# Kernel tuning notes

Hardware: AMD Instinct MI355X
Metric: run time of the kernel (lower is better)

The kernel has to match this reference:

```python
import jax, jax.numpy as jnp
import numpy as np


def setup_inputs() -> dict:
    key = jax.random.key(0)
    ks = jax.random.split(key, 7)
    T, B, D, H, F = 1024, 128, 256, 256, 128
    inputs = jax.random.normal(ks[0], (T, B, D), dtype=jnp.float32)
    # stacked gate linears (forget, input, update, output): [D+H, 4H]
    Wg = jax.random.normal(ks[1], (D + H, 4 * H), dtype=jnp.float32) / np.sqrt(D + H)
    bg = jax.random.normal(ks[2], (4 * H,), dtype=jnp.float32) * 0.01
    # stacked per-gate FFNs: Linear(H->F), ReLU, Linear(F->H), sigmoid/tanh
    W1 = jax.random.normal(ks[3], (4, H, F), dtype=jnp.float32) / np.sqrt(H)
    b1 = jax.random.normal(ks[4], (4, F), dtype=jnp.float32) * 0.01
    W2 = jax.random.normal(ks[5], (4, F, H), dtype=jnp.float32) / np.sqrt(F)
    b2 = jax.random.normal(ks[6], (4, H), dtype=jnp.float32) * 0.01
    return {"inputs": inputs, "Wg": Wg, "bg": bg, "W1": W1, "b1": b1, "W2": W2, "b2": b2}


def reference(inputs, Wg, bg, W1, b1, W2, b2):
    T, B, D = inputs.shape
    H = W2.shape[-1]

    def step(carry, x):
        hx, cx = carry
        comb = jnp.concatenate([x, hx], axis=1)              # [B, D+H]
        z = (comb @ Wg + bg).reshape(B, 4, H)                # stacked gate linears
        z = jnp.transpose(z, (1, 0, 2))                      # [4, B, H]
        h1 = jax.nn.relu(jnp.einsum('gbh,ghf->gbf', z, W1) + b1[:, None, :])
        z2 = jnp.einsum('gbf,gfh->gbh', h1, W2) + b2[:, None, :]  # [4, B, H]
        f = jax.nn.sigmoid(z2[0])
        i = jax.nn.sigmoid(z2[1])
        g = jnp.tanh(z2[2])
        o = jax.nn.sigmoid(z2[3])
        cx = f * cx + i * g
        hx = o * jnp.tanh(cx)
        return (hx, cx), hx

    h0 = jnp.zeros((B, H), dtype=inputs.dtype)
    c0 = jnp.zeros((B, H), dtype=inputs.dtype)
    (hx, cx), outputs = jax.lax.scan(step, (h0, c0), inputs)
    return outputs, (hx, cx)
```

## Files before the change

### kernel.cpp

```cpp
#include <hip/hip_runtime.h>
#include <hip/hip_fp16.h>
#include <cstdint>

#define T_STEPS 1024
#define BATCH   128
#define DIM     256
#define HID     256
#define FF      128
#define CHUNK   16

typedef _Float16 h2 __attribute__((ext_vector_type(2)));

#define WGXP_OFF 0
#define WGHP_OFF 262144
#define W1P_OFF  524288
#define W2P_OFF  655360
#define WS_HALFS 786432
#define EX_BYTE_OFF 1572864
#define EX_WORDS    262144
#define WS_SPLIT4_BYTES (EX_BYTE_OFF + EX_WORDS * 4)

#define KEEPU4(v) asm volatile("" : "+v"((v).x), "+v"((v).y), "+v"((v).z), "+v"((v).w))

__device__ __forceinline__ float sigmoidf_(float x) {
    return 1.0f / (1.0f + __expf(-x));
}
__device__ __forceinline__ float tanhf_(float x) {
    float e = __expf(2.0f * x);
    return 1.0f - 2.0f / (e + 1.0f);
}
__device__ __forceinline__ float fdot2_(h2 a, h2 b, float c) {
#if __has_builtin(__builtin_amdgcn_fdot2)
    return __builtin_amdgcn_fdot2(a, b, c, false);
#else
    return fmaf((float)a.x, (float)b.x, fmaf((float)a.y, (float)b.y, c));
#endif
}

union U4H { uint4 u; h2 h[4]; };
union HU  { unsigned short u; _Float16 h; };

__global__ __launch_bounds__(256)
void convert_kernel(const float* __restrict__ Wg,
                    const float* __restrict__ W1,
                    const float* __restrict__ W2,
                    _Float16* __restrict__ ws)
{
    int i = blockIdx.x * 256 + threadIdx.x;
    if (i < 524288) {
        int k = i >> 10, c = i & 1023;
        if (k < 256) {
            ws[WGXP_OFF + (((size_t)(k >> 3) << 10) + c) * 8 + (k & 7)] = (_Float16)Wg[i];
        } else {
            int k2 = k - 256;
            ws[WGHP_OFF + (((size_t)(k2 >> 3) << 10) + c) * 8 + (k2 & 7)] = (_Float16)Wg[i];
        }
    } else if (i < 655360) {
        int j = i - 524288;
        int g = j >> 15, k = (j >> 7) & 255, f = j & 127;
        ws[W1P_OFF + (((size_t)((g << 5) + (k >> 3)) << 7) + f) * 8 + (k & 7)] = (_Float16)W1[j];
    } else if (i < 786432) {
        int j = i - 655360;
        int g = j >> 15, f = (j >> 8) & 127, h = j & 255;
        ws[W2P_OFF + (((size_t)((g << 4) + (f >> 3)) << 8) + h) * 8 + (f & 7)] = (_Float16)W2[j];
    }
}

__global__ __launch_bounds__(512)
void exinit_kernel(unsigned* __restrict__ ex) {
    int i = blockIdx.x * 512 + threadIdx.x;
    if (i < EX_WORDS) ex[i] = 0u;
}

__global__ __launch_bounds__(512, 1)
void qlstm_split4r_kernel(const float* __restrict__ x,
                          const _Float16* __restrict__ ws,
                          unsigned* ex,
                          const float* __restrict__ bg,
                          const float* __restrict__ b1,
                          const float* __restrict__ b2,
                          float* __restrict__ out)
{
    const int blk = blockIdx.x;
    const int g   = blk >> 6;
    const int bp  = blk & 63;
    const int tid = threadIdx.x;

    __shared__ __align__(16) _Float16 xc[2 * CHUNK * DIM];
    __shared__ __align__(16) _Float16 zxc[2 * CHUNK * 256];
    __shared__ __align__(16) _Float16 ch2buf[512];
    __shared__ __align__(16) _Float16 zh[512];
    __shared__ __align__(16) _Float16 h1h[256];
    __shared__ float pbuf[1024];
    __shared__ float bgs[256], b2s[256], b1s[128];

    if (tid < 256) {
        bgs[tid] = bg[(g << 8) + tid];
        b2s[tid] = b2[(g << 8) + tid];
    }
    if (tid < 128) b1s[tid] = b1[(g << 7) + tid];
    ch2buf[tid] = (_Float16)0.0f;
    float c_reg = 0.0f;

    const uint4* __restrict__ wgxp = reinterpret_cast<const uint4*>(ws + WGXP_OFF);
    const uint4* __restrict__ wghp = reinterpret_cast<const uint4*>(ws + WGHP_OFF);
    const uint4* __restrict__ w1p  = reinterpret_cast<const uint4*>(ws + W1P_OFF);
    const uint4* __restrict__ w2p  = reinterpret_cast<const uint4*>(ws + W2P_OFF);

    const int cc   = tid & 255;
    const int kh16 = (tid >> 8) << 4;
    const int kq8  = ((tid >> 7) & 3) << 3;
    const int ffi  = tid & 127;
    const int fh8  = (tid >> 8) << 3;

    uint4 wgh_r[16], w1_r[8], w2_r[8];
    #pragma unroll
    for (int j = 0; j < 16; ++j) wgh_r[j] = wghp[((kh16 + j) << 10) + (g << 8) + cc];
    #pragma unroll
    for (int j = 0; j < 8; ++j)  w1_r[j]  = w1p[(((g << 5) + kq8 + j) << 7) + ffi];
    #pragma unroll
    for (int j = 0; j < 8; ++j)  w2_r[j]  = w2p[(((g << 4) + fh8 + j) << 8) + cc];
    #pragma unroll
    for (int j = 0; j < 16; ++j) KEEPU4(wgh_r[j]);
    #pragma unroll
    for (int j = 0; j < 8; ++j)  KEEPU4(w1_r[j]);
    #pragma unroll
    for (int j = 0; j < 8; ++j)  KEEPU4(w2_r[j]);

    __syncthreads();

    for (int t0 = 0; t0 < T_STEPS; t0 += CHUNK) {
        #pragma unroll
        for (int j = 0; j < 4; ++j) {
            int i4 = j * 512 + tid;
            int bl = i4 >> 10, rem = i4 & 1023, tl = rem >> 6, d4 = rem & 63;
            float4 v = reinterpret_cast<const float4*>(
                x + ((size_t)(t0 + tl) * BATCH + bp + (bl << 6)) * DIM)[d4];
            int base = bl * 4096 + tl * 256 + (d4 << 2);
            xc[base + 0] = (_Float16)v.x;
            xc[base + 1] = (_Float16)v.y;
            xc[base + 2] = (_Float16)v.z;
            xc[base + 3] = (_Float16)v.w;
        }
        __syncthreads();

        {
            const int th = tid >> 8;
            const U4H* xcv = reinterpret_cast<const U4H*>(xc);
            float acc[2][8];
            #pragma unroll
            for (int bl = 0; bl < 2; ++bl)
                #pragma unroll
                for (int j = 0; j < 8; ++j) acc[bl][j] = bgs[cc];
            for (int k8 = 0; k8 < 32; ++k8) {
                U4H w; w.u = wgxp[(k8 << 10) + (g << 8) + cc];
                #pragma unroll
                for (int bl = 0; bl < 2; ++bl) {
                    #pragma unroll
                    for (int j = 0; j < 8; ++j) {
                        U4H xv; xv.u = xcv[bl * 512 + (th * 8 + j) * 32 + k8].u;
                        acc[bl][j] = fdot2_(xv.h[0], w.h[0], acc[bl][j]);
                        acc[bl][j] = fdot2_(xv.h[1], w.h[1], acc[bl][j]);
                        acc[bl][j] = fdot2_(xv.h[2], w.h[2], acc[bl][j]);
                        acc[bl][j] = fdot2_(xv.h[3], w.h[3], acc[bl][j]);
                    }
                }
            }
            #pragma unroll
            for (int bl = 0; bl < 2; ++bl)
                #pragma unroll
                for (int j = 0; j < 8; ++j)
                    zxc[bl * 4096 + (th * 8 + j) * 256 + cc] = (_Float16)acc[bl][j];
        }
        __syncthreads();

        for (int tc = 0; tc < CHUNK; ++tc) {
            const int s = t0 + tc;

            {
                const uint4* hA4 = reinterpret_cast<const uint4*>(ch2buf);
                const uint4* hB4 = reinterpret_cast<const uint4*>(ch2buf + 256);
                float aA = 0.0f, aB = 0.0f;
                #pragma unroll
                for (int j = 0; j < 16; ++j) {
                    const int k8 = kh16 + j;
                    U4H w;  w.u  = wgh_r[j];
                    U4H ha; ha.u = hA4[k8];
                    U4H hb; hb.u = hB4[k8];
                    aA = fdot2_(ha.h[0], w.h[0], aA);
                    aA = fdot2_(ha.h[1], w.h[1], aA);
                    aA = fdot2_(ha.h[2], w.h[2], aA);
                    aA = fdot2_(ha.h[3], w.h[3], aA);
                    aB = fdot2_(hb.h[0], w.h[0], aB);
                    aB = fdot2_(hb.h[1], w.h[1], aB);
                    aB = fdot2_(hb.h[2], w.h[2], aB);
                    aB = fdot2_(hb.h[3], w.h[3], aB);
                }
                pbuf[tid] = aA;
                pbuf[512 + tid] = aB;
            }
            __syncthreads();
            {
                const int bl = tid >> 8, c = tid & 255;
                float z = (float)zxc[bl * 4096 + tc * 256 + c]
                        + pbuf[bl * 512 + c] + pbuf[bl * 512 + 256 + c];
                zh[bl * 256 + c] = (_Float16)z;
            }
            __syncthreads();

            {
                const uint4* zA4 = reinterpret_cast<const uint4*>(zh);
                const uint4* zB4 = reinterpret_cast<const uint4*>(zh + 256);
                float aA = 0.0f, aB = 0.0f;
                #pragma unroll
                for (int j = 0; j < 8; ++j) {
                    const int k8 = kq8 + j;
                    U4H w;  w.u  = w1_r[j];
                    U4H za; za.u = zA4[k8];
                    U4H zb; zb.u = zB4[k8];
                    aA = fdot2_(za.h[0], w.h[0], aA);
                    aA = fdot2_(za.h[1], w.h[1], aA);
                    aA = fdot2_(za.h[2], w.h[2], aA);
                    aA = fdot2_(za.h[3], w.h[3], aA);
                    aB = fdot2_(zb.h[0], w.h[0], aB);
                    aB = fdot2_(zb.h[1], w.h[1], aB);
                    aB = fdot2_(zb.h[2], w.h[2], aB);
                    aB = fdot2_(zb.h[3], w.h[3], aB);
                }
                pbuf[tid] = aA;
                pbuf[512 + tid] = aB;
            }
            __syncthreads();
            if (tid < 256) {
                const int bl = tid >> 7, f = tid & 127;
                float v = b1s[f] + pbuf[bl * 512 + f] + pbuf[bl * 512 + 128 + f]
                                 + pbuf[bl * 512 + 256 + f] + pbuf[bl * 512 + 384 + f];
                h1h[bl * 128 + f] = (_Float16)fmaxf(v, 0.0f);
            }
            __syncthreads();

            {
                const uint4* pA4 = reinterpret_cast<const uint4*>(h1h);
                const uint4* pB4 = reinterpret_cast<const uint4*>(h1h + 128);
                float aA = 0.0f, aB = 0.0f;
                #pragma unroll
                for (int j = 0; j < 8; ++j) {
                    const int f8 = fh8 + j;
                    U4H w;  w.u  = w2_r[j];
                    U4H ha; ha.u = pA4[f8];
                    U4H hb; hb.u = pB4[f8];
                    aA = fdot2_(ha.h[0], w.h[0], aA);
                    aA = fdot2_(ha.h[1], w.h[1], aA);
                    aA = fdot2_(ha.h[2], w.h[2], aA);
                    aA = fdot2_(ha.h[3], w.h[3], aA);
                    aB = fdot2_(hb.h[0], w.h[0], aB);
                    aB = fdot2_(hb.h[1], w.h[1], aB);
                    aB = fdot2_(hb.h[2], w.h[2], aB);
                    aB = fdot2_(hb.h[3], w.h[3], aB);
                }
                pbuf[tid] = aA;
                pbuf[512 + tid] = aB;
            }
            __syncthreads();

            {
                const int bl = tid >> 8, c = tid & 255;
                const int b  = bp + (bl << 6);
                float z2 = b2s[c] + pbuf[bl * 512 + c] + pbuf[bl * 512 + 256 + c];
                HU hu; hu.h = (_Float16)z2;
                unsigned word = ((unsigned)(s + 1) << 16) | (unsigned)hu.u;
                unsigned widx = (unsigned)(b * 2048 + g * 512 + ((s & 1) << 8) + c);
                __hip_atomic_store(&ex[widx], word, __ATOMIC_RELAXED, __HIP_MEMORY_SCOPE_AGENT);

                const unsigned base = (unsigned)(b * 2048 + ((s & 1) << 8) + c);
                const unsigned want = (unsigned)(s + 1) << 16;
                unsigned w0, w1, w2, w3;
                for (;;) {
                    w0 = __hip_atomic_load(&ex[base],        __ATOMIC_RELAXED, __HIP_MEMORY_SCOPE_AGENT);
                    w1 = __hip_atomic_load(&ex[base + 512],  __ATOMIC_RELAXED, __HIP_MEMORY_SCOPE_AGENT);
                    w2 = __hip_atomic_load(&ex[base + 1024], __ATOMIC_RELAXED, __HIP_MEMORY_SCOPE_AGENT);
                    w3 = __hip_atomic_load(&ex[base + 1536], __ATOMIC_RELAXED, __HIP_MEMORY_SCOPE_AGENT);
                    unsigned m = ((w0 ^ want) | (w1 ^ want) | (w2 ^ want) | (w3 ^ want)) & 0xFFFF0000u;
                    if (m == 0u) break;
                    __builtin_amdgcn_s_sleep(1);
                }
                HU hf, hi, hg, ho;
                hf.u = (unsigned short)(w0 & 0xFFFFu);
                hi.u = (unsigned short)(w1 & 0xFFFFu);
                hg.u = (unsigned short)(w2 & 0xFFFFu);
                ho.u = (unsigned short)(w3 & 0xFFFFu);
                float fg = sigmoidf_((float)hf.h);
                float ig = sigmoidf_((float)hi.h);
                float gg = tanhf_((float)hg.h);
                float og = sigmoidf_((float)ho.h);
                c_reg = fmaf(fg, c_reg, ig * gg);
                float hh = og * tanhf_(c_reg);
                ch2buf[bl * 256 + c] = (_Float16)hh;
                if (g == 0) {
                    out[((size_t)s * BATCH + b) * HID + c] = hh;
                    if (s == T_STEPS - 1) {
                        const size_t TBH = (size_t)T_STEPS * BATCH * HID;
                        out[TBH + (size_t)b * HID + c] = hh;
                        out[TBH + (size_t)BATCH * HID + (size_t)b * HID + c] = c_reg;
                    }
                }
            }
            __syncthreads();
        }
    }
}

__global__ __launch_bounds__(1024)
void qlstm_chunk_kernel(const float* __restrict__ x,
                        const _Float16* __restrict__ ws,
                        const float* __restrict__ bg,
                        const float* __restrict__ b1,
                        const float* __restrict__ b2,
                        float* __restrict__ out)
{
    const int b   = blockIdx.x;
    const int tid = threadIdx.x;

    __shared__ __align__(16) _Float16 xc[CHUNK * DIM];
    __shared__ __align__(16) _Float16 zxc[CHUNK * 1024];
    __shared__ __align__(16) _Float16 zh[1024];
    __shared__ __align__(16) _Float16 h1h[512];
    __shared__ __align__(16) _Float16 ch2buf[HID];
    __shared__ float z2buf[1024];
    __shared__ float cbuf[HID];
    __shared__ float hbuf[HID];

    const float rbg = bg[tid];
    const float rb1 = (tid < 512) ? b1[tid] : 0.0f;
    const float rb2 = b2[tid];

    if (tid < HID) { cbuf[tid] = 0.0f; hbuf[tid] = 0.0f; ch2buf[tid] = (_Float16)0.0f; }

    const uint4* __restrict__ wgxp = reinterpret_cast<const uint4*>(ws + WGXP_OFF);
    const uint4* __restrict__ wghp = reinterpret_cast<const uint4*>(ws + WGHP_OFF);
    const uint4* __restrict__ w1p  = reinterpret_cast<const uint4*>(ws + W1P_OFF);
    const uint4* __restrict__ w2p  = reinterpret_cast<const uint4*>(ws + W2P_OFF);
    const h2* ch2 = reinterpret_cast<const h2*>(ch2buf);
    const U4H* xcv = reinterpret_cast<const U4H*>(xc);

    for (int t0 = 0; t0 < T_STEPS; t0 += CHUNK) {
        #pragma unroll
        for (int j = 0; j < (CHUNK * DIM) / 1024; ++j) {
            int idx = tid + j * 1024;
            int tl = idx >> 8, d = idx & 255;
            xc[tl * DIM + d] = (_Float16)x[((size_t)(t0 + tl) * BATCH + b) * DIM + d];
        }
        __syncthreads();

        {
            float acc[CHUNK];
            #pragma unroll
            for (int tc = 0; tc < CHUNK; ++tc) acc[tc] = rbg;
            for (int k8 = 0; k8 < DIM / 8; ++k8) {
                U4H w; w.u = wgxp[(k8 << 10) + tid];
                #pragma unroll
                for (int tc = 0; tc < CHUNK; ++tc) {
                    U4H xv; xv.u = xcv[tc * (DIM / 8) + k8].u;
                    acc[tc] = fdot2_(xv.h[0], w.h[0], acc[tc]);
                    acc[tc] = fdot2_(xv.h[1], w.h[1], acc[tc]);
                    acc[tc] = fdot2_(xv.h[2], w.h[2], acc[tc]);
                    acc[tc] = fdot2_(xv.h[3], w.h[3], acc[tc]);
                }
            }
            #pragma unroll
            for (int tc = 0; tc < CHUNK; ++tc) zxc[tc * 1024 + tid] = (_Float16)acc[tc];
        }
        __syncthreads();

        for (int tc = 0; tc < CHUNK; ++tc) {
            {
                float acc = (float)zxc[tc * 1024 + tid];
                #pragma unroll 8
                for (int k8 = 0; k8 < HID / 8; ++k8) {
                    U4H w; w.u = wghp[(k8 << 10) + tid];
                    acc = fdot2_(ch2[4 * k8 + 0], w.h[0], acc);
                    acc = fdot2_(ch2[4 * k8 + 1], w.h[1], acc);
                    acc = fdot2_(ch2[4 * k8 + 2], w.h[2], acc);
                    acc = fdot2_(ch2[4 * k8 + 3], w.h[3], acc);
                }
                zh[tid] = (_Float16)acc;
            }
            __syncthreads();

            if (tid < 512) {
                const int g = tid >> 7, f = tid & 127;
                const h2* zp = reinterpret_cast<const h2*>(zh + (g << 8));
                float acc = rb1;
                #pragma unroll 8
                for (int k8 = 0; k8 < HID / 8; ++k8) {
                    U4H w; w.u = w1p[(((g << 5) + k8) << 7) + f];
                    acc = fdot2_(zp[4 * k8 + 0], w.h[0], acc);
                    acc = fdot2_(zp[4 * k8 + 1], w.h[1], acc);
                    acc = fdot2_(zp[4 * k8 + 2], w.h[2], acc);
                    acc = fdot2_(zp[4 * k8 + 3], w.h[3], acc);
                }
                h1h[tid] = (_Float16)fmaxf(acc, 0.0f);
            }
            __syncthreads();

            {
                const int g = tid >> 8, hcol = tid & 255;
                const h2* hp = reinterpret_cast<const h2*>(h1h + (g << 7));
                float acc = rb2;
                #pragma unroll 8
                for (int f8 = 0; f8 < FF / 8; ++f8) {
                    U4H w; w.u = w2p[(((g << 4) + f8) << 8) + hcol];
                    acc = fdot2_(hp[4 * f8 + 0], w.h[0], acc);
                    acc = fdot2_(hp[4 * f8 + 1], w.h[1], acc);
                    acc = fdot2_(hp[4 * f8 + 2], w.h[2], acc);
                    acc = fdot2_(hp[4 * f8 + 3], w.h[3], acc);
                }
                z2buf[tid] = acc;
            }
            __syncthreads();

            if (tid < HID) {
                float zf = z2buf[tid];
                float zi = z2buf[HID + tid];
                float zg = z2buf[2 * HID + tid];
                float zo = z2buf[3 * HID + tid];
                float fg = sigmoidf_(zf);
                float ig = sigmoidf_(zi);
                float gg = tanhf_(zg);
                float og = sigmoidf_(zo);
                float cc = fmaf(fg, cbuf[tid], ig * gg);
                float hh = og * tanhf_(cc);
                cbuf[tid] = cc;
                hbuf[tid] = hh;
                ch2buf[tid] = (_Float16)hh;
                out[((size_t)(t0 + tc) * BATCH + b) * HID + tid] = hh;
            }
            __syncthreads();
        }
    }

    if (tid < HID) {
        const size_t TBH = (size_t)T_STEPS * BATCH * HID;
        out[TBH + (size_t)b * HID + tid] = hbuf[tid];
        out[TBH + (size_t)BATCH * HID + (size_t)b * HID + tid] = cbuf[tid];
    }
}

extern "C" void kernel_launch(void* const* d_in, const int* in_sizes, int n_in,
                              void* d_out, int out_size, void* d_ws, size_t ws_size,
                              hipStream_t stream) {
    const float* x  = (const float*)d_in[0];
    const float* Wg = (const float*)d_in[1];
    const float* bg = (const float*)d_in[2];
    const float* W1 = (const float*)d_in[3];
    const float* b1 = (const float*)d_in[4];
    const float* W2 = (const float*)d_in[5];
    const float* b2 = (const float*)d_in[6];
    float* out = (float*)d_out;
    char* wsc = (char*)d_ws;

    if (ws_size >= (size_t)WS_SPLIT4_BYTES) {
        _Float16* ws = (_Float16*)wsc;
        unsigned* ex = (unsigned*)(wsc + EX_BYTE_OFF);
        convert_kernel<<<WS_HALFS / 256, 256, 0, stream>>>(Wg, W1, W2, ws);
        exinit_kernel<<<EX_WORDS / 512, 512, 0, stream>>>(ex);
        qlstm_split4r_kernel<<<256, 512, 0, stream>>>(x, ws, ex, bg, b1, b2, out);
    } else if (ws_size >= (size_t)WS_HALFS * sizeof(_Float16)) {
        _Float16* ws = (_Float16*)wsc;
        convert_kernel<<<WS_HALFS / 256, 256, 0, stream>>>(Wg, W1, W2, ws);
        qlstm_chunk_kernel<<<BATCH, 1024, 0, stream>>>(x, ws, bg, b1, b2, out);
    }
}
```

Measured before the change: 3.759 ms.

## Remap blocks so batch groups share an XCD and add volatile fast-path exchange

Blocks are remapped so the four gate blocks for a given batch pair land in the same XCD group (blk&7), which keeps cross-block exchange traffic inside one XCD's L2. A second exchange buffer is written and polled with plain volatile loads for up to 64 tries, falling back to agent-scope atomic loads on the original buffer if that times out. This aims to cut per-step handshake latency between the cooperating blocks. The cost is doubled exchange memory and init work, and it relies on volatile loads seeing writes made by other CUs in the same XCD.

```diff
diff --git a/kernel.cpp b/kernel.cpp
--- a/kernel.cpp
+++ b/kernel.cpp
@@ -18,7 +18,9 @@
 #define WS_HALFS 786432
 #define EX_BYTE_OFF 1572864
 #define EX_WORDS    262144
+#define FP_BYTE_OFF (EX_BYTE_OFF + EX_WORDS * 4)
 #define WS_SPLIT4_BYTES (EX_BYTE_OFF + EX_WORDS * 4)
+#define WS_FP_BYTES     (FP_BYTE_OFF + EX_WORDS * 4)
 
 #define KEEPU4(v) asm volatile("" : "+v"((v).x), "+v"((v).y), "+v"((v).z), "+v"((v).w))
 
@@ -67,24 +69,27 @@
 }
 
 __global__ __launch_bounds__(512)
-void exinit_kernel(unsigned* __restrict__ ex) {
+void exinit_kernel(unsigned* __restrict__ ex, int nwords) {
     int i = blockIdx.x * 512 + threadIdx.x;
-    if (i < EX_WORDS) ex[i] = 0u;
+    if (i < nwords) ex[i] = 0u;
 }
 
 __global__ __launch_bounds__(512, 1)
 void qlstm_split4r_kernel(const float* __restrict__ x,
                           const _Float16* __restrict__ ws,
                           unsigned* ex,
+                          unsigned* fp,
                           const float* __restrict__ bg,
                           const float* __restrict__ b1,
                           const float* __restrict__ b2,
                           float* __restrict__ out)
 {
-    const int blk = blockIdx.x;
-    const int g   = blk >> 6;
-    const int bp  = blk & 63;
-    const int tid = threadIdx.x;
+    const int blk  = blockIdx.x;
+    const int xcdg = blk & 7;
+    const int q    = blk >> 3;
+    const int g    = q & 3;
+    const int bp   = (xcdg << 3) | (q >> 2);
+    const int tid  = threadIdx.x;
 
     __shared__ __align__(16) _Float16 xc[2 * CHUNK * DIM];
     __shared__ __align__(16) _Float16 zxc[2 * CHUNK * 256];
@@ -101,6 +106,8 @@
     if (tid < 128) b1s[tid] = b1[(g << 7) + tid];
     ch2buf[tid] = (_Float16)0.0f;
     float c_reg = 0.0f;
+    bool use_fast = (fp != nullptr);
+    volatile unsigned* fpv = fp;
 
     const uint4* __restrict__ wgxp = reinterpret_cast<const uint4*>(ws + WGXP_OFF);
     const uint4* __restrict__ wghp = reinterpret_cast<const uint4*>(ws + WGHP_OFF);
@@ -270,19 +277,35 @@
                 HU hu; hu.h = (_Float16)z2;
                 unsigned word = ((unsigned)(s + 1) << 16) | (unsigned)hu.u;
                 unsigned widx = (unsigned)(b * 2048 + g * 512 + ((s & 1) << 8) + c);
+                if (fp) fpv[widx] = word;
                 __hip_atomic_store(&ex[widx], word, __ATOMIC_RELAXED, __HIP_MEMORY_SCOPE_AGENT);
 
                 const unsigned base = (unsigned)(b * 2048 + ((s & 1) << 8) + c);
                 const unsigned want = (unsigned)(s + 1) << 16;
                 unsigned w0, w1, w2, w3;
-                for (;;) {
-                    w0 = __hip_atomic_load(&ex[base],        __ATOMIC_RELAXED, __HIP_MEMORY_SCOPE_AGENT);
-                    w1 = __hip_atomic_load(&ex[base + 512],  __ATOMIC_RELAXED, __HIP_MEMORY_SCOPE_AGENT);
-                    w2 = __hip_atomic_load(&ex[base + 1024], __ATOMIC_RELAXED, __HIP_MEMORY_SCOPE_AGENT);
-                    w3 = __hip_atomic_load(&ex[base + 1536], __ATOMIC_RELAXED, __HIP_MEMORY_SCOPE_AGENT);
-                    unsigned m = ((w0 ^ want) | (w1 ^ want) | (w2 ^ want) | (w3 ^ want)) & 0xFFFF0000u;
-                    if (m == 0u) break;
-                    __builtin_amdgcn_s_sleep(1);
+                bool got = false;
+                if (use_fast) {
+                    for (int it = 0; it < 64; ++it) {
+                        w0 = fpv[base];
+                        w1 = fpv[base + 512];
+                        w2 = fpv[base + 1024];
+                        w3 = fpv[base + 1536];
+                        unsigned m = ((w0 ^ want) | (w1 ^ want) | (w2 ^ want) | (w3 ^ want)) & 0xFFFF0000u;
+                        if (m == 0u) { got = true; break; }
+                        __builtin_amdgcn_s_sleep(1);
+                    }
+                    if (!got) use_fast = false;
+                }
+                if (!got) {
+                    for (;;) {
+                        w0 = __hip_atomic_load(&ex[base],        __ATOMIC_RELAXED, __HIP_MEMORY_SCOPE_AGENT);
+                        w1 = __hip_atomic_load(&ex[base + 512],  __ATOMIC_RELAXED, __HIP_MEMORY_SCOPE_AGENT);
+                        w2 = __hip_atomic_load(&ex[base + 1024], __ATOMIC_RELAXED, __HIP_MEMORY_SCOPE_AGENT);
+                        w3 = __hip_atomic_load(&ex[base + 1536], __ATOMIC_RELAXED, __HIP_MEMORY_SCOPE_AGENT);
+                        unsigned m = ((w0 ^ want) | (w1 ^ want) | (w2 ^ want) | (w3 ^ want)) & 0xFFFF0000u;
+                        if (m == 0u) break;
+                        __builtin_amdgcn_s_sleep(1);
+                    }
                 }
                 HU hf, hi, hg, ho;
                 hf.u = (unsigned short)(w0 & 0xFFFFu);
@@ -344,9 +367,7 @@
     const U4H* xcv = reinterpret_cast<const U4H*>(xc);
 
     for (int t0 = 0; t0 < T_STEPS; t0 += CHUNK) {
-        #pragma unroll
-        for (int j = 0; j < (CHUNK * DIM) / 1024; ++j) {
-            int idx = tid + j * 1024;
+        for (int idx = tid; idx < CHUNK * DIM; idx += 1024) {
             int tl = idx >> 8, d = idx & 255;
             xc[tl * DIM + d] = (_Float16)x[((size_t)(t0 + tl) * BATCH + b) * DIM + d];
         }
@@ -428,9 +449,9 @@
                 float ig = sigmoidf_(zi);
                 float gg = tanhf_(zg);
                 float og = sigmoidf_(zo);
-                float cc = fmaf(fg, cbuf[tid], ig * gg);
-                float hh = og * tanhf_(cc);
-                cbuf[tid] = cc;
+                float ccv = fmaf(fg, cbuf[tid], ig * gg);
+                float hh = og * tanhf_(ccv);
+                cbuf[tid] = ccv;
                 hbuf[tid] = hh;
                 ch2buf[tid] = (_Float16)hh;
                 out[((size_t)(t0 + tc) * BATCH + b) * HID + tid] = hh;
@@ -462,9 +483,12 @@
     if (ws_size >= (size_t)WS_SPLIT4_BYTES) {
         _Float16* ws = (_Float16*)wsc;
         unsigned* ex = (unsigned*)(wsc + EX_BYTE_OFF);
+        unsigned* fp = (ws_size >= (size_t)WS_FP_BYTES) ? (unsigned*)(wsc + FP_BYTE_OFF)
+                                                        : nullptr;
+        int nwords = fp ? (EX_WORDS * 2) : EX_WORDS;
         convert_kernel<<<WS_HALFS / 256, 256, 0, stream>>>(Wg, W1, W2, ws);
-        exinit_kernel<<<EX_WORDS / 512, 512, 0, stream>>>(ex);
-        qlstm_split4r_kernel<<<256, 512, 0, stream>>>(x, ws, ex, bg, b1, b2, out);
+        exinit_kernel<<<(nwords + 511) / 512, 512, 0, stream>>>(ex, nwords);
+        qlstm_split4r_kernel<<<256, 512, 0, stream>>>(x, ws, ex, fp, bg, b1, b2, out);
     } else if (ws_size >= (size_t)WS_HALFS * sizeof(_Float16)) {
         _Float16* ws = (_Float16*)wsc;
         convert_kernel<<<WS_HALFS / 256, 256, 0, stream>>>(Wg, W1, W2, ws);
```

Result: slower. 5.131 ms (+36.5%).
